# Optimization experiments

Measured on AMD Instinct MI355X. Metric: run time of the kernel, lower is better.

The kernel has to match this reference:

```python
import jax, jax.numpy as jnp
import numpy as np

N_NODES = 384
HEIGHT = 60
LN_EPS = 1e-5


def setup_inputs() -> dict:
    key = jax.random.key(0)
    ks = jax.random.split(key, 6)
    C = 256
    E = 3072
    x = jax.random.normal(ks[0], (N_NODES, C, HEIGHT), dtype=jnp.float32)
    edge_attr = jax.random.normal(ks[1], (E, 5), dtype=jnp.float32)
    edge_index = jax.random.randint(ks[2], (2, E), 0, N_NODES)
    W_edge = jax.random.normal(ks[3], (5, C), dtype=jnp.float32) * 0.3
    b_edge = jnp.zeros((C,), dtype=jnp.float32)
    W_conv = jax.random.normal(ks[4], (C, 3 * C), dtype=jnp.float32) * (1.0 / np.sqrt(3 * C))
    ln_gamma = jnp.ones((C, HEIGHT), dtype=jnp.float32)
    ln_beta = jnp.zeros((C, HEIGHT), dtype=jnp.float32)
    return {"x": x, "edge_attr": edge_attr, "edge_index": edge_index,
            "W_edge": W_edge, "b_edge": b_edge, "W_conv": W_conv,
            "ln_gamma": ln_gamma, "ln_beta": ln_beta}


def reference(x, edge_attr, edge_index, W_edge, b_edge, W_conv, ln_gamma, ln_beta):
    # x: (N, C, 60); PyG convention: edge_index[0]=source (j), edge_index[1]=target (i)
    C = x.shape[1]
    src, dst = edge_index[0], edge_index[1]
    h_i = x[dst]                    # (E, C, 60) gather target features
    h_j = x[src]                    # (E, C, 60) gather source features
    ea = edge_attr @ W_edge + b_edge            # (E, C) edge Linear
    ea = jnp.broadcast_to(ea[:, :, None], h_i.shape)  # repeat over height
    h = jnp.concatenate([h_i, h_j - h_i, ea], axis=1)  # (E, 3C, 60)
    # Conv1d kernel_size=1, bias=False -> channel contraction
    m = jnp.einsum('ech,oc->eoh', h, W_conv)    # (E, C, 60)
    # LayerNorm over (C, 60) per edge
    mu = jnp.mean(m, axis=(1, 2), keepdims=True)
    var = jnp.var(m, axis=(1, 2), keepdims=True)
    m = (m - mu) * jax.lax.rsqrt(var + LN_EPS) * ln_gamma + ln_beta
    m = jax.nn.relu(m)
    # aggr='add' scatter into target nodes
    out = jax.ops.segment_sum(m.reshape(m.shape[0], C * HEIGHT), dst,
                              num_segments=N_NODES)
    return out.reshape(N_NODES, C, HEIGHT)
```

## Files before the change

### kernel.cpp

```cpp
#include <hip/hip_runtime.h>

#define N_NODES 384
#define CCH 256
#define HT 60
#define CH (CCH*HT)
#define CH4 (CH/4)
#define LN_EPS 1e-5f
#define KSPLIT 40

typedef __attribute__((ext_vector_type(8))) short bf16x8;
typedef __attribute__((ext_vector_type(4))) float f32x4;

__device__ inline unsigned short f2bf(float f) {
    unsigned int u = __float_as_uint(f);
    unsigned int r = (u + 0x7FFF + ((u >> 16) & 1)) >> 16;
    return (unsigned short)r;
}
__device__ inline float bf2f(unsigned short u) {
    return __uint_as_float(((unsigned int)u) << 16);
}

__global__ __launch_bounds__(1024) void k_setup(const float* __restrict__ Wc,
                                                unsigned short* __restrict__ Wfrag) {
    int idx = blockIdx.x * 1024 + threadIdx.x;
    int j = idx & 7, lane = (idx >> 3) & 63, ks = (idx >> 9) & 7, mt = idx >> 12;
    int o = mt * 16 + (lane & 15);
    int c = ks * 32 + (lane >> 4) * 8 + j;
    float v;
    if (o < 256) v = Wc[o * 768 + c] - Wc[o * 768 + 256 + c];
    else         v = Wc[(o - 256) * 768 + 256 + c];
    Wfrag[idx] = f2bf(v);
}

__global__ __launch_bounds__(256) void k_node_mfma(const float* __restrict__ x,
                                                   const unsigned short* __restrict__ Wfrag,
                                                   unsigned short* __restrict__ Abf,
                                                   unsigned short* __restrict__ Bbf) {
    __shared__ unsigned short xT[32 * 256];
    int n = blockIdx.x, half = blockIdx.y, tid = threadIdx.x;

    const float4* xg = (const float4*)(x + (size_t)n * CH);
    if (half == 0) {
        for (int i = tid; i < 2048; i += 256) {
            int c = i >> 3, jj = i & 7;
            int r0 = jj * 4;
            float4 v = xg[c * 15 + jj];
            xT[(r0+0) * 256 + (c ^ (((r0+0) & 7) << 3))] = f2bf(v.x);
            xT[(r0+1) * 256 + (c ^ (((r0+1) & 7) << 3))] = f2bf(v.y);
            xT[(r0+2) * 256 + (c ^ (((r0+2) & 7) << 3))] = f2bf(v.z);
            xT[(r0+3) * 256 + (c ^ (((r0+3) & 7) << 3))] = f2bf(v.w);
        }
    } else {
        for (int i = tid; i < 4 * 256; i += 256) {
            int r = 28 + (i >> 8), c = i & 255;
            xT[r * 256 + (c ^ ((r & 7) << 3))] = 0;
        }
        for (int i = tid; i < 1792; i += 256) {
            int c = i / 7, jj = i - c * 7;
            int r0 = jj * 4;
            float4 v = xg[c * 15 + 8 + jj];
            xT[(r0+0) * 256 + (c ^ (((r0+0) & 7) << 3))] = f2bf(v.x);
            xT[(r0+1) * 256 + (c ^ (((r0+1) & 7) << 3))] = f2bf(v.y);
            xT[(r0+2) * 256 + (c ^ (((r0+2) & 7) << 3))] = f2bf(v.z);
            xT[(r0+3) * 256 + (c ^ (((r0+3) & 7) << 3))] = f2bf(v.w);
        }
    }
    __syncthreads();

    int w = tid >> 6, lane = tid & 63;
    int l15 = lane & 15, lg = lane >> 4;

    f32x4 acc[8][2];
#pragma unroll
    for (int mt = 0; mt < 8; ++mt)
#pragma unroll
        for (int nt = 0; nt < 2; ++nt)
            acc[mt][nt] = (f32x4){0.f, 0.f, 0.f, 0.f};

    const unsigned short* wbase = Wfrag + ((size_t)(w * 8) * 8) * 64 * 8;
    for (int ks = 0; ks < 8; ++ks) {
        bf16x8 bfr[2];
#pragma unroll
        for (int nt = 0; nt < 2; ++nt) {
            int row = nt * 16 + l15;
            int col = ks * 32 + lg * 8;
            int idx = row * 256 + (col ^ ((row & 7) << 3));
            bfr[nt] = *(const bf16x8*)(&xT[idx]);
        }
#pragma unroll
        for (int mt = 0; mt < 8; ++mt) {
            const bf16x8 afr = *(const bf16x8*)(wbase + (((size_t)mt * 8 + ks) * 64 + lane) * 8);
#pragma unroll
            for (int nt = 0; nt < 2; ++nt)
                acc[mt][nt] = __builtin_amdgcn_mfma_f32_16x16x32_bf16(afr, bfr[nt], acc[mt][nt], 0, 0, 0);
        }
    }

#pragma unroll
    for (int mt = 0; mt < 8; ++mt) {
        int mtg = w * 8 + mt;
        int obase = mtg * 16 + 4 * lg;
        unsigned short* dst0 = (obase < 256)
            ? (Abf + (size_t)n * CH + (size_t)obase * 60)
            : (Bbf + (size_t)n * CH + (size_t)(obase - 256) * 60);
#pragma unroll
        for (int nt = 0; nt < 2; ++nt) {
            int h = half * 32 + nt * 16 + l15;
            if (h < 60) {
#pragma unroll
                for (int r = 0; r < 4; ++r)
                    dst0[r * 60 + h] = f2bf(acc[mt][nt][r]);
            }
        }
    }
}

__global__ __launch_bounds__(256) void k_gramscal(const unsigned short* __restrict__ Abf,
                                                  const unsigned short* __restrict__ Bbf,
                                                  const float* __restrict__ Wc,
                                                  const float* __restrict__ We,
                                                  const float* __restrict__ be,
                                                  const int* __restrict__ dst, int E,
                                                  float* __restrict__ Gpart,
                                                  float* __restrict__ RAB,
                                                  float4* __restrict__ Sc,
                                                  float* __restrict__ M,
                                                  float* __restrict__ bias0,
                                                  int* __restrict__ offs,
                                                  int* __restrict__ elist) {
    int b = blockIdx.x;
    int tid = threadIdx.x, w = tid >> 6, lane = tid & 63;
    int l15 = lane & 15, lg = lane >> 4;
    if (b == 0) {
        __shared__ int cnt[N_NODES];
        __shared__ int sc0[N_NODES], sc1[N_NODES];
        for (int i = tid; i < N_NODES; i += 256) cnt[i] = 0;
        __syncthreads();
        for (int e = tid; e < E; e += 256) atomicAdd(&cnt[dst[e]], 1);
        __syncthreads();
        for (int i = tid; i < N_NODES; i += 256) sc0[i] = cnt[i];
        __syncthreads();
        int flip = 0;
        for (int d = 1; d < N_NODES; d <<= 1) {
            const int* s_ = flip ? sc1 : sc0;
            int* d_ = flip ? sc0 : sc1;
            for (int i = tid; i < N_NODES; i += 256)
                d_[i] = s_[i] + (i >= d ? s_[i - d] : 0);
            __syncthreads();
            flip ^= 1;
        }
        const int* pos = flip ? sc1 : sc0;
        for (int i = tid; i < N_NODES; i += 256) {
            offs[i + 1] = pos[i];
            cnt[i] = (i == 0) ? 0 : pos[i - 1];
        }
        if (tid == 0) offs[0] = 0;
        __syncthreads();
        for (int e = tid; e < E; e += 256) {
            int d = dst[e];
            elist[atomicAdd(&cnt[d], 1)] = e;
        }
        __syncthreads();
        for (int n2 = tid; n2 < N_NODES; n2 += 256) {
            int lo = (n2 == 0) ? 0 : pos[n2 - 1], hi = pos[n2];
            for (int i = lo + 1; i < hi; ++i) {
                int key = elist[i]; int j = i - 1;
                while (j >= lo && elist[j] > key) { elist[j + 1] = elist[j]; --j; }
                elist[j + 1] = key;
            }
        }
        return;
    }
    if (b == 1) {
        int o = tid;
        float m0=0,m1=0,m2=0,m3=0,m4=0,bb=0;
        for (int k = 0; k < 256; ++k) {
            float w3 = Wc[o * 768 + 512 + k];
            m0 += We[0*256+k] * w3;
            m1 += We[1*256+k] * w3;
            m2 += We[2*256+k] * w3;
            m3 += We[3*256+k] * w3;
            m4 += We[4*256+k] * w3;
            bb += be[k] * w3;
        }
        M[0*256+o]=m0; M[1*256+o]=m1; M[2*256+o]=m2; M[3*256+o]=m3; M[4*256+o]=m4;
        bias0[o] = bb;
        return;
    }
    if (b < 362) {
        int g = b - 2;
        int ks = g / 9, rem = g - ks * 9, bi = rem % 3, bj = rem / 3;
        int d0 = bi * 128 + (w & 1) * 64;
        int s0 = bj * 128 + (w >> 1) * 64;
        int ksbase = ks * 384 + lg * 8;

        const unsigned short* Ap[4];
        const unsigned short* Bp[4];
#pragma unroll
        for (int t = 0; t < 4; ++t) {
            Ap[t] = Abf + (size_t)(d0 + t * 16 + l15) * CH + ksbase;
            Bp[t] = Bbf + (size_t)(s0 + t * 16 + l15) * CH + ksbase;
        }

        f32x4 acc[4][4];
#pragma unroll
        for (int a = 0; a < 4; ++a)
#pragma unroll
            for (int bb = 0; bb < 4; ++bb) acc[a][bb] = (f32x4){0.f,0.f,0.f,0.f};

        bf16x8 a0[4], b0[4], a1[4], b1[4];
#pragma unroll
        for (int t = 0; t < 4; ++t) {
            a0[t] = *(const bf16x8*)(Ap[t]);
            b0[t] = *(const bf16x8*)(Bp[t]);
        }
#pragma unroll
        for (int kk = 0; kk < 12; kk += 2) {
            if (kk + 1 < 12) {
#pragma unroll
                for (int t = 0; t < 4; ++t) {
                    a1[t] = *(const bf16x8*)(Ap[t] + (kk + 1) * 32);
                    b1[t] = *(const bf16x8*)(Bp[t] + (kk + 1) * 32);
                }
            }
#pragma unroll
            for (int a = 0; a < 4; ++a)
#pragma unroll
                for (int bb = 0; bb < 4; ++bb)
                    acc[a][bb] = __builtin_amdgcn_mfma_f32_16x16x32_bf16(a0[a], b0[bb], acc[a][bb], 0, 0, 0);
            if (kk + 2 < 12) {
#pragma unroll
                for (int t = 0; t < 4; ++t) {
                    a0[t] = *(const bf16x8*)(Ap[t] + (kk + 2) * 32);
                    b0[t] = *(const bf16x8*)(Bp[t] + (kk + 2) * 32);
                }
            }
#pragma unroll
            for (int a = 0; a < 4; ++a)
#pragma unroll
                for (int bb = 0; bb < 4; ++bb)
                    acc[a][bb] = __builtin_amdgcn_mfma_f32_16x16x32_bf16(a1[a], b1[bb], acc[a][bb], 0, 0, 0);
        }

        float* gp = Gpart + (size_t)ks * 384 * 384;
#pragma unroll
        for (int a = 0; a < 4; ++a)
#pragma unroll
            for (int bb = 0; bb < 4; ++bb) {
                int d = d0 + a * 16 + 4 * lg;
                int s = s0 + bb * 16 + l15;
#pragma unroll
                for (int r = 0; r < 4; ++r)
                    gp[(size_t)(d + r) * 384 + s] = acc[a][bb][r];
            }
    } else {
        __shared__ float red[16];
        int n = b - 362;
        const ushort4* Ab = (const ushort4*)(Abf + (size_t)n * CH + tid * 60);
        const ushort4* Bb = (const ushort4*)(Bbf + (size_t)n * CH + tid * 60);
        float rsA = 0.f, qA = 0.f, rsB = 0.f, qB = 0.f;
#pragma unroll
        for (int i = 0; i < 15; ++i) {
            ushort4 a = Ab[i], bb2 = Bb[i];
#pragma unroll
            for (int j = 0; j < 4; ++j) {
                float va = bf2f(((const unsigned short*)&a)[j]);
                float vb = bf2f(((const unsigned short*)&bb2)[j]);
                rsA += va; qA += va * va;
                rsB += vb; qB += vb * vb;
            }
        }
        RAB[(size_t)n * 512 + tid] = rsA;
        RAB[(size_t)n * 512 + 256 + tid] = rsB;
        float sA = rsA, sB = rsB;
#pragma unroll
        for (int o = 32; o >= 1; o >>= 1) {
            sA += __shfl_xor(sA, o, 64); qA += __shfl_xor(qA, o, 64);
            sB += __shfl_xor(sB, o, 64); qB += __shfl_xor(qB, o, 64);
        }
        if (lane == 0) { red[w*4]=sA; red[w*4+1]=qA; red[w*4+2]=sB; red[w*4+3]=qB; }
        __syncthreads();
        if (tid == 0) {
            Sc[n] = make_float4(red[0]+red[4]+red[8]+red[12],
                                red[1]+red[5]+red[9]+red[13],
                                red[2]+red[6]+red[10]+red[14],
                                red[3]+red[7]+red[11]+red[15]);
        }
    }
}

__global__ __launch_bounds__(256) void k_stats2(const float* __restrict__ ea,
                                                const float* __restrict__ M,
                                                const float* __restrict__ bias0,
                                                const int* __restrict__ srcA,
                                                const int* __restrict__ dstA, int E,
                                                const float* __restrict__ RAB,
                                                const float4* __restrict__ Sc,
                                                const float* __restrict__ Gpart,
                                                float* __restrict__ cbuf,
                                                float2* __restrict__ stats) {
    int w = threadIdx.x >> 6, lane = threadIdx.x & 63;
    int e = blockIdx.x * 4 + w;
    if (e >= E) return;
    int s = srcA[e], d = dstA[e];
    float ev0 = ea[e*5], ev1 = ea[e*5+1], ev2 = ea[e*5+2], ev3 = ea[e*5+3], ev4 = ea[e*5+4];
    float sc = 0.f, sc2 = 0.f, dots = 0.f;
#pragma unroll
    for (int r = 0; r < 4; ++r) {
        int o = lane + 64 * r;
        float c = bias0[o] + ev0*M[o] + ev1*M[256+o] + ev2*M[512+o] + ev3*M[768+o] + ev4*M[1024+o];
        cbuf[(size_t)e * 256 + o] = c;
        sc += c; sc2 += c * c;
        dots += (RAB[(size_t)d * 512 + o] + RAB[(size_t)s * 512 + 256 + o]) * c;
    }
    float g = (lane < KSPLIT) ? Gpart[((size_t)lane * 384 + d) * 384 + s] : 0.f;
#pragma unroll
    for (int o2 = 32; o2 >= 1; o2 >>= 1) {
        sc   += __shfl_xor(sc, o2, 64);
        sc2  += __shfl_xor(sc2, o2, 64);
        dots += __shfl_xor(dots, o2, 64);
        g    += __shfl_xor(g, o2, 64);
    }
    if (lane == 0) {
        float4 scd = Sc[d], scs = Sc[s];
        float S1 = scd.x + scs.z + 60.f * sc;
        float S2 = scd.y + scs.w + 60.f * sc2 + 2.f * (g + dots);
        float mu = S1 * (1.0f / (float)CH);
        float var = S2 * (1.0f / (float)CH) - mu * mu;
        stats[e] = make_float2(mu, rsqrtf(var + LN_EPS));
    }
}

__global__ __launch_bounds__(256) void k_apply(const unsigned short* __restrict__ Abf,
                                               const unsigned short* __restrict__ Bbf,
                                               const float* __restrict__ cbuf,
                                               const float2* __restrict__ stats,
                                               const int* __restrict__ srcArr,
                                               const int* __restrict__ offsets,
                                               const int* __restrict__ elist,
                                               const float* __restrict__ gamma,
                                               const float* __restrict__ beta,
                                               float* __restrict__ out) {
    int b = blockIdx.x;
    int xcd = b & 7;
    int cg = xcd >> 1;
    int n = ((b >> 3) << 1) | (xcd & 1);
    int tid = threadIdx.x;
    size_t sbase = (size_t)n * CH + (size_t)cg * 3840;
    const ushort4* Ab = (const ushort4*)(Abf + sbase);
    const float4*  g4 = (const float4*)(gamma + (size_t)cg * 3840);
    const float4*  b4 = (const float4*)(beta  + (size_t)cg * 3840);

    float4 af[4], gv[4], bv[4], acc[4];
    int ci[4];
#pragma unroll
    for (int r = 0; r < 4; ++r) {
        acc[r] = make_float4(0.f, 0.f, 0.f, 0.f);
        af[r] = make_float4(0.f, 0.f, 0.f, 0.f);
        gv[r] = make_float4(0.f, 0.f, 0.f, 0.f);
        bv[r] = make_float4(0.f, 0.f, 0.f, 0.f);
        ci[r] = 0;
    }
#pragma unroll
    for (int r = 0; r < 4; ++r) {
        if (r < 3 || tid < 192) {
            int i = tid + 256 * r;
            ci[r] = i / 15;
            ushort4 aw = Ab[i];
            af[r].x = bf2f(aw.x); af[r].y = bf2f(aw.y);
            af[r].z = bf2f(aw.z); af[r].w = bf2f(aw.w);
            gv[r] = g4[i];
            bv[r] = b4[i];
        }
    }

    int lo = offsets[n], hi = offsets[n + 1];
    int k = lo;
    for (; k + 1 < hi; k += 2) {
        int e0 = elist[k], e1 = elist[k + 1];
        int s0 = srcArr[e0], s1 = srcArr[e1];
        float2 st0 = stats[e0], st1 = stats[e1];
        const ushort4* B0 = (const ushort4*)(Bbf + (size_t)s0 * CH + (size_t)cg * 3840);
        const ushort4* B1 = (const ushort4*)(Bbf + (size_t)s1 * CH + (size_t)cg * 3840);
        const float* c0 = cbuf + (size_t)e0 * 256 + cg * 64;
        const float* c1 = cbuf + (size_t)e1 * 256 + cg * 64;
#pragma unroll
        for (int r = 0; r < 4; ++r) {
            if (r < 3 || tid < 192) {
                int i = tid + 256 * r;
                ushort4 bw0 = B0[i];
                ushort4 bw1 = B1[i];
                float cc0 = c0[ci[r]];
                float cc1 = c1[ci[r]];
                float m0x = af[r].x + bf2f(bw0.x) + cc0;
                float m0y = af[r].y + bf2f(bw0.y) + cc0;
                float m0z = af[r].z + bf2f(bw0.z) + cc0;
                float m0w = af[r].w + bf2f(bw0.w) + cc0;
                float m1x = af[r].x + bf2f(bw1.x) + cc1;
                float m1y = af[r].y + bf2f(bw1.y) + cc1;
                float m1z = af[r].z + bf2f(bw1.z) + cc1;
                float m1w = af[r].w + bf2f(bw1.w) + cc1;
                acc[r].x += fmaxf((m0x - st0.x) * st0.y * gv[r].x + bv[r].x, 0.f);
                acc[r].y += fmaxf((m0y - st0.x) * st0.y * gv[r].y + bv[r].y, 0.f);
                acc[r].z += fmaxf((m0z - st0.x) * st0.y * gv[r].z + bv[r].z, 0.f);
                acc[r].w += fmaxf((m0w - st0.x) * st0.y * gv[r].w + bv[r].w, 0.f);
                acc[r].x += fmaxf((m1x - st1.x) * st1.y * gv[r].x + bv[r].x, 0.f);
                acc[r].y += fmaxf((m1y - st1.x) * st1.y * gv[r].y + bv[r].y, 0.f);
                acc[r].z += fmaxf((m1z - st1.x) * st1.y * gv[r].z + bv[r].z, 0.f);
                acc[r].w += fmaxf((m1w - st1.x) * st1.y * gv[r].w + bv[r].w, 0.f);
            }
        }
    }
    if (k < hi) {
        int e = elist[k];
        int s = srcArr[e];
        float2 st = stats[e];
        const ushort4* Bb = (const ushort4*)(Bbf + (size_t)s * CH + (size_t)cg * 3840);
        const float* cc = cbuf + (size_t)e * 256 + cg * 64;
#pragma unroll
        for (int r = 0; r < 4; ++r) {
            if (r < 3 || tid < 192) {
                int i = tid + 256 * r;
                float ccv = cc[ci[r]];
                ushort4 bw = Bb[i];
                float mx = af[r].x + bf2f(bw.x) + ccv;
                float my = af[r].y + bf2f(bw.y) + ccv;
                float mz = af[r].z + bf2f(bw.z) + ccv;
                float mw = af[r].w + bf2f(bw.w) + ccv;
                acc[r].x += fmaxf((mx - st.x) * st.y * gv[r].x + bv[r].x, 0.f);
                acc[r].y += fmaxf((my - st.x) * st.y * gv[r].y + bv[r].y, 0.f);
                acc[r].z += fmaxf((mz - st.x) * st.y * gv[r].z + bv[r].z, 0.f);
                acc[r].w += fmaxf((mw - st.x) * st.y * gv[r].w + bv[r].w, 0.f);
            }
        }
    }
    float4* ob = (float4*)(out + sbase);
#pragma unroll
    for (int r = 0; r < 4; ++r)
        if (r < 3 || tid < 192) ob[tid + 256 * r] = acc[r];
}

extern "C" void kernel_launch(void* const* d_in, const int* in_sizes, int n_in,
                              void* d_out, int out_size, void* d_ws, size_t ws_size,
                              hipStream_t stream) {
    const float* x     = (const float*)d_in[0];
    const float* ea    = (const float*)d_in[1];
    const int*   ei    = (const int*)d_in[2];
    const float* We    = (const float*)d_in[3];
    const float* be    = (const float*)d_in[4];
    const float* Wc    = (const float*)d_in[5];
    const float* gamma = (const float*)d_in[6];
    const float* beta  = (const float*)d_in[7];
    const int E = in_sizes[2] / 2;
    const int* src = ei;
    const int* dst = ei + E;

    char* ws = (char*)d_ws;
    size_t off = 0;
    auto alloc = [&](size_t bytes) -> void* {
        void* p = ws + off;
        off += (bytes + 255) & ~(size_t)255;
        return p;
    };
    unsigned short* Abf    = (unsigned short*)alloc((size_t)N_NODES * CH * 2);
    unsigned short* Bbf    = (unsigned short*)alloc((size_t)N_NODES * CH * 2);
    float*          cbuf   = (float*)alloc((size_t)E * 256 * 4);
    float2*         stats  = (float2*)alloc((size_t)E * 8);
    unsigned short* Wfrag  = (unsigned short*)alloc(512 * 256 * 2);
    float*          M      = (float*)alloc(5 * 256 * 4);
    float*          bias0  = (float*)alloc(256 * 4);
    float*          RAB    = (float*)alloc((size_t)N_NODES * 512 * 4);
    float4*         Sc     = (float4*)alloc((size_t)N_NODES * 16);
    float*          Gpart  = (float*)alloc((size_t)KSPLIT * 384 * 384 * 4);
    int*            offs   = (int*)alloc((N_NODES + 1) * 4);
    int*            elist  = (int*)alloc((size_t)E * 4);

    k_setup<<<128, 1024, 0, stream>>>(Wc, Wfrag);
    k_node_mfma<<<dim3(N_NODES, 2), 256, 0, stream>>>(x, Wfrag, Abf, Bbf);
    k_gramscal<<<746, 256, 0, stream>>>(Abf, Bbf, Wc, We, be, dst, E,
                                        Gpart, RAB, Sc, M, bias0, offs, elist);
    k_stats2<<<(E + 3) / 4, 256, 0, stream>>>(ea, M, bias0, src, dst, E, RAB, Sc, Gpart,
                                              cbuf, stats);
    k_apply<<<N_NODES * 4, 256, 0, stream>>>(Abf, Bbf, cbuf, stats, src, offs, elist,
                                             gamma, beta, (float*)d_out);
}
```

Before: 91.71 us.

## Fuse per-edge LayerNorm stats computation into apply kernel via shared-memory chunks

Removes the separate k_stats2 launch and its cbuf/stats global buffers; each apply block now computes per-edge mean/rstd and the edge-linear channel values for chunks of 32 incoming edges into shared memory before accumulating. This saves a kernel launch and global round trips. In exchange, the stats work is done redundantly by each of the four channel-group blocks per node, and a block barrier is added per chunk.

```diff
diff --git a/kernel.cpp b/kernel.cpp
--- a/kernel.cpp
+++ b/kernel.cpp
@@ -7,6 +7,7 @@
 #define CH4 (CH/4)
 #define LN_EPS 1e-5f
 #define KSPLIT 40
+#define ECHUNK 32
 
 typedef __attribute__((ext_vector_type(8))) short bf16x8;
 typedef __attribute__((ext_vector_type(4))) float f32x4;
@@ -289,63 +290,27 @@
     }
 }
 
-__global__ __launch_bounds__(256) void k_stats2(const float* __restrict__ ea,
-                                                const float* __restrict__ M,
-                                                const float* __restrict__ bias0,
-                                                const int* __restrict__ srcA,
-                                                const int* __restrict__ dstA, int E,
-                                                const float* __restrict__ RAB,
-                                                const float4* __restrict__ Sc,
-                                                const float* __restrict__ Gpart,
-                                                float* __restrict__ cbuf,
-                                                float2* __restrict__ stats) {
-    int w = threadIdx.x >> 6, lane = threadIdx.x & 63;
-    int e = blockIdx.x * 4 + w;
-    if (e >= E) return;
-    int s = srcA[e], d = dstA[e];
-    float ev0 = ea[e*5], ev1 = ea[e*5+1], ev2 = ea[e*5+2], ev3 = ea[e*5+3], ev4 = ea[e*5+4];
-    float sc = 0.f, sc2 = 0.f, dots = 0.f;
-#pragma unroll
-    for (int r = 0; r < 4; ++r) {
-        int o = lane + 64 * r;
-        float c = bias0[o] + ev0*M[o] + ev1*M[256+o] + ev2*M[512+o] + ev3*M[768+o] + ev4*M[1024+o];
-        cbuf[(size_t)e * 256 + o] = c;
-        sc += c; sc2 += c * c;
-        dots += (RAB[(size_t)d * 512 + o] + RAB[(size_t)s * 512 + 256 + o]) * c;
-    }
-    float g = (lane < KSPLIT) ? Gpart[((size_t)lane * 384 + d) * 384 + s] : 0.f;
-#pragma unroll
-    for (int o2 = 32; o2 >= 1; o2 >>= 1) {
-        sc   += __shfl_xor(sc, o2, 64);
-        sc2  += __shfl_xor(sc2, o2, 64);
-        dots += __shfl_xor(dots, o2, 64);
-        g    += __shfl_xor(g, o2, 64);
-    }
-    if (lane == 0) {
-        float4 scd = Sc[d], scs = Sc[s];
-        float S1 = scd.x + scs.z + 60.f * sc;
-        float S2 = scd.y + scs.w + 60.f * sc2 + 2.f * (g + dots);
-        float mu = S1 * (1.0f / (float)CH);
-        float var = S2 * (1.0f / (float)CH) - mu * mu;
-        stats[e] = make_float2(mu, rsqrtf(var + LN_EPS));
-    }
-}
-
 __global__ __launch_bounds__(256) void k_apply(const unsigned short* __restrict__ Abf,
                                                const unsigned short* __restrict__ Bbf,
-                                               const float* __restrict__ cbuf,
-                                               const float2* __restrict__ stats,
+                                               const float* __restrict__ ea,
+                                               const float* __restrict__ M,
+                                               const float* __restrict__ bias0,
                                                const int* __restrict__ srcArr,
                                                const int* __restrict__ offsets,
                                                const int* __restrict__ elist,
+                                               const float* __restrict__ RAB,
+                                               const float4* __restrict__ Sc,
+                                               const float* __restrict__ Gpart,
                                                const float* __restrict__ gamma,
                                                const float* __restrict__ beta,
                                                float* __restrict__ out) {
+    __shared__ float2 stl[ECHUNK];
+    __shared__ float  cl[ECHUNK][64];
     int b = blockIdx.x;
     int xcd = b & 7;
     int cg = xcd >> 1;
     int n = ((b >> 3) << 1) | (xcd & 1);
-    int tid = threadIdx.x;
+    int tid = threadIdx.x, w = tid >> 6, lane = tid & 63;
     size_t sbase = (size_t)n * CH + (size_t)cg * 3840;
     const ushort4* Ab = (const ushort4*)(Abf + sbase);
     const float4*  g4 = (const float4*)(gamma + (size_t)cg * 3840);
@@ -375,62 +340,101 @@
     }
 
     int lo = offsets[n], hi = offsets[n + 1];
-    int k = lo;
-    for (; k + 1 < hi; k += 2) {
-        int e0 = elist[k], e1 = elist[k + 1];
-        int s0 = srcArr[e0], s1 = srcArr[e1];
-        float2 st0 = stats[e0], st1 = stats[e1];
-        const ushort4* B0 = (const ushort4*)(Bbf + (size_t)s0 * CH + (size_t)cg * 3840);
-        const ushort4* B1 = (const ushort4*)(Bbf + (size_t)s1 * CH + (size_t)cg * 3840);
-        const float* c0 = cbuf + (size_t)e0 * 256 + cg * 64;
-        const float* c1 = cbuf + (size_t)e1 * 256 + cg * 64;
-#pragma unroll
-        for (int r = 0; r < 4; ++r) {
-            if (r < 3 || tid < 192) {
-                int i = tid + 256 * r;
-                ushort4 bw0 = B0[i];
-                ushort4 bw1 = B1[i];
-                float cc0 = c0[ci[r]];
-                float cc1 = c1[ci[r]];
-                float m0x = af[r].x + bf2f(bw0.x) + cc0;
-                float m0y = af[r].y + bf2f(bw0.y) + cc0;
-                float m0z = af[r].z + bf2f(bw0.z) + cc0;
-                float m0w = af[r].w + bf2f(bw0.w) + cc0;
-                float m1x = af[r].x + bf2f(bw1.x) + cc1;
-                float m1y = af[r].y + bf2f(bw1.y) + cc1;
-                float m1z = af[r].z + bf2f(bw1.z) + cc1;
-                float m1w = af[r].w + bf2f(bw1.w) + cc1;
-                acc[r].x += fmaxf((m0x - st0.x) * st0.y * gv[r].x + bv[r].x, 0.f);
-                acc[r].y += fmaxf((m0y - st0.x) * st0.y * gv[r].y + bv[r].y, 0.f);
-                acc[r].z += fmaxf((m0z - st0.x) * st0.y * gv[r].z + bv[r].z, 0.f);
-                acc[r].w += fmaxf((m0w - st0.x) * st0.y * gv[r].w + bv[r].w, 0.f);
-                acc[r].x += fmaxf((m1x - st1.x) * st1.y * gv[r].x + bv[r].x, 0.f);
-                acc[r].y += fmaxf((m1y - st1.x) * st1.y * gv[r].y + bv[r].y, 0.f);
-                acc[r].z += fmaxf((m1z - st1.x) * st1.y * gv[r].z + bv[r].z, 0.f);
-                acc[r].w += fmaxf((m1w - st1.x) * st1.y * gv[r].w + bv[r].w, 0.f);
-            }
-        }
-    }
-    if (k < hi) {
-        int e = elist[k];
-        int s = srcArr[e];
-        float2 st = stats[e];
-        const ushort4* Bb = (const ushort4*)(Bbf + (size_t)s * CH + (size_t)cg * 3840);
-        const float* cc = cbuf + (size_t)e * 256 + cg * 64;
-#pragma unroll
-        for (int r = 0; r < 4; ++r) {
-            if (r < 3 || tid < 192) {
-                int i = tid + 256 * r;
-                float ccv = cc[ci[r]];
-                ushort4 bw = Bb[i];
-                float mx = af[r].x + bf2f(bw.x) + ccv;
-                float my = af[r].y + bf2f(bw.y) + ccv;
-                float mz = af[r].z + bf2f(bw.z) + ccv;
-                float mw = af[r].w + bf2f(bw.w) + ccv;
-                acc[r].x += fmaxf((mx - st.x) * st.y * gv[r].x + bv[r].x, 0.f);
-                acc[r].y += fmaxf((my - st.x) * st.y * gv[r].y + bv[r].y, 0.f);
-                acc[r].z += fmaxf((mz - st.x) * st.y * gv[r].z + bv[r].z, 0.f);
-                acc[r].w += fmaxf((mw - st.x) * st.y * gv[r].w + bv[r].w, 0.f);
+    for (int base = lo; base < hi; base += ECHUNK) {
+        int cnt = min(ECHUNK, hi - base);
+        if (base != lo) __syncthreads();
+        for (int kk = w; kk < cnt; kk += 4) {
+            int e = elist[base + kk];
+            int s = srcArr[e];
+            float ev0 = ea[e*5], ev1 = ea[e*5+1], ev2 = ea[e*5+2],
+                  ev3 = ea[e*5+3], ev4 = ea[e*5+4];
+            float sc = 0.f, sc2 = 0.f, dots = 0.f;
+            float csave = 0.f;
+#pragma unroll
+            for (int r = 0; r < 4; ++r) {
+                int o = lane + 64 * r;
+                float c = bias0[o] + ev0*M[o] + ev1*M[256+o] + ev2*M[512+o]
+                        + ev3*M[768+o] + ev4*M[1024+o];
+                if (r == cg) csave = c;
+                sc += c; sc2 += c * c;
+                dots += (RAB[(size_t)n * 512 + o] + RAB[(size_t)s * 512 + 256 + o]) * c;
+            }
+            cl[kk][lane] = csave;
+            float g = (lane < KSPLIT) ? Gpart[((size_t)lane * 384 + n) * 384 + s] : 0.f;
+#pragma unroll
+            for (int o2 = 32; o2 >= 1; o2 >>= 1) {
+                sc   += __shfl_xor(sc, o2, 64);
+                sc2  += __shfl_xor(sc2, o2, 64);
+                dots += __shfl_xor(dots, o2, 64);
+                g    += __shfl_xor(g, o2, 64);
+            }
+            if (lane == 0) {
+                float4 scd = Sc[n], scs = Sc[s];
+                float S1 = scd.x + scs.z + 60.f * sc;
+                float S2 = scd.y + scs.w + 60.f * sc2 + 2.f * (g + dots);
+                float mu = S1 * (1.0f / (float)CH);
+                float var = S2 * (1.0f / (float)CH) - mu * mu;
+                stl[kk] = make_float2(mu, rsqrtf(var + LN_EPS));
+            }
+        }
+        __syncthreads();
+        int k = 0;
+        for (; k + 1 < cnt; k += 2) {
+            int e0 = elist[base + k], e1 = elist[base + k + 1];
+            int s0 = srcArr[e0], s1 = srcArr[e1];
+            float2 st0 = stl[k], st1 = stl[k + 1];
+            const ushort4* B0 = (const ushort4*)(Bbf + (size_t)s0 * CH + (size_t)cg * 3840);
+            const ushort4* B1 = (const ushort4*)(Bbf + (size_t)s1 * CH + (size_t)cg * 3840);
+            const float* c0 = cl[k];
+            const float* c1 = cl[k + 1];
+#pragma unroll
+            for (int r = 0; r < 4; ++r) {
+                if (r < 3 || tid < 192) {
+                    int i = tid + 256 * r;
+                    ushort4 bw0 = B0[i];
+                    ushort4 bw1 = B1[i];
+                    float cc0 = c0[ci[r]];
+                    float cc1 = c1[ci[r]];
+                    float m0x = af[r].x + bf2f(bw0.x) + cc0;
+                    float m0y = af[r].y + bf2f(bw0.y) + cc0;
+                    float m0z = af[r].z + bf2f(bw0.z) + cc0;
+                    float m0w = af[r].w + bf2f(bw0.w) + cc0;
+                    float m1x = af[r].x + bf2f(bw1.x) + cc1;
+                    float m1y = af[r].y + bf2f(bw1.y) + cc1;
+                    float m1z = af[r].z + bf2f(bw1.z) + cc1;
+                    float m1w = af[r].w + bf2f(bw1.w) + cc1;
+                    acc[r].x += fmaxf((m0x - st0.x) * st0.y * gv[r].x + bv[r].x, 0.f);
+                    acc[r].y += fmaxf((m0y - st0.x) * st0.y * gv[r].y + bv[r].y, 0.f);
+                    acc[r].z += fmaxf((m0z - st0.x) * st0.y * gv[r].z + bv[r].z, 0.f);
+                    acc[r].w += fmaxf((m0w - st0.x) * st0.y * gv[r].w + bv[r].w, 0.f);
+                    acc[r].x += fmaxf((m1x - st1.x) * st1.y * gv[r].x + bv[r].x, 0.f);
+                    acc[r].y += fmaxf((m1y - st1.x) * st1.y * gv[r].y + bv[r].y, 0.f);
+                    acc[r].z += fmaxf((m1z - st1.x) * st1.y * gv[r].z + bv[r].z, 0.f);
+                    acc[r].w += fmaxf((m1w - st1.x) * st1.y * gv[r].w + bv[r].w, 0.f);
+                }
+            }
+        }
+        if (k < cnt) {
+            int e = elist[base + k];
+            int s = srcArr[e];
+            float2 st = stl[k];
+            const ushort4* Bb = (const ushort4*)(Bbf + (size_t)s * CH + (size_t)cg * 3840);
+            const float* cc = cl[k];
+#pragma unroll
+            for (int r = 0; r < 4; ++r) {
+                if (r < 3 || tid < 192) {
+                    int i = tid + 256 * r;
+                    float ccv = cc[ci[r]];
+                    ushort4 bw = Bb[i];
+                    float mx = af[r].x + bf2f(bw.x) + ccv;
+                    float my = af[r].y + bf2f(bw.y) + ccv;
+                    float mz = af[r].z + bf2f(bw.z) + ccv;
+                    float mw = af[r].w + bf2f(bw.w) + ccv;
+                    acc[r].x += fmaxf((mx - st.x) * st.y * gv[r].x + bv[r].x, 0.f);
+                    acc[r].y += fmaxf((my - st.x) * st.y * gv[r].y + bv[r].y, 0.f);
+                    acc[r].z += fmaxf((mz - st.x) * st.y * gv[r].z + bv[r].z, 0.f);
+                    acc[r].w += fmaxf((mw - st.x) * st.y * gv[r].w + bv[r].w, 0.f);
+                }
             }
         }
     }
@@ -464,8 +468,6 @@
     };
     unsigned short* Abf    = (unsigned short*)alloc((size_t)N_NODES * CH * 2);
     unsigned short* Bbf    = (unsigned short*)alloc((size_t)N_NODES * CH * 2);
-    float*          cbuf   = (float*)alloc((size_t)E * 256 * 4);
-    float2*         stats  = (float2*)alloc((size_t)E * 8);
     unsigned short* Wfrag  = (unsigned short*)alloc(512 * 256 * 2);
     float*          M      = (float*)alloc(5 * 256 * 4);
     float*          bias0  = (float*)alloc(256 * 4);
@@ -479,8 +481,6 @@
     k_node_mfma<<<dim3(N_NODES, 2), 256, 0, stream>>>(x, Wfrag, Abf, Bbf);
     k_gramscal<<<746, 256, 0, stream>>>(Abf, Bbf, Wc, We, be, dst, E,
                                         Gpart, RAB, Sc, M, bias0, offs, elist);
-    k_stats2<<<(E + 3) / 4, 256, 0, stream>>>(ea, M, bias0, src, dst, E, RAB, Sc, Gpart,
-                                              cbuf, stats);
-    k_apply<<<N_NODES * 4, 256, 0, stream>>>(Abf, Bbf, cbuf, stats, src, offs, elist,
-                                             gamma, beta, (float*)d_out);
-}
+    k_apply<<<N_NODES * 4, 256, 0, stream>>>(Abf, Bbf, ea, M, bias0, src, offs, elist,
+                                             RAB, Sc, Gpart, gamma, beta, (float*)d_out);
+}
```

Measured after the change: 99.58 us. 8.6% more time.
